# Kernel tuning notes

Hardware: AMD Instinct MI355X
Metric: run time of the kernel (lower is better)

The kernel has to match this reference:

```python
import jax, jax.numpy as jnp
import numpy as np

BITS = 8
EPS = 1e-08


def _scalar_quantize_maxabs(x, scale, bits, eps):
    # clamp(round(x / scale), -qmax, qmax) with a fixed (precomputed) scalar scale
    qmax = float(2 ** (bits - 1) - 1)
    s = jnp.maximum(scale, eps)
    return jnp.clip(jnp.round(x / s), -qmax, qmax)


def setup_inputs() -> dict:
    key = jax.random.key(0)
    k1, k2, k3 = jax.random.split(key, 3)
    B, S, D_in, D_out = 4, 2048, 2048, 2048
    hidden_states = jax.random.normal(k1, (B, S, D_in), dtype=jnp.float32)
    # weight_quantized holds low-bit integer values stored as float (as produced by the quantizer)
    qmax = float(2 ** (BITS - 1) - 1)
    weight_quantized = jnp.round(
        jnp.clip(jax.random.normal(k2, (D_in, D_out), dtype=jnp.float32) * (qmax / 3.0), -qmax, qmax)
    )
    x_scale = jnp.asarray(0.05, dtype=jnp.float32)
    bias = jax.random.normal(k3, (D_out,), dtype=jnp.float32)
    return {
        "hidden_states": hidden_states,
        "weight_quantized": weight_quantized,
        "x_scale": x_scale,
        "bias": bias,
    }


def reference(hidden_states, weight_quantized, x_scale, bias) -> jnp.ndarray:
    original_shape = hidden_states.shape[:-1]
    input_dim = hidden_states.shape[-1]
    x_flat = hidden_states.reshape(-1, input_dim)  # [B*S, D_in]
    x_q = _scalar_quantize_maxabs(x_flat, x_scale.reshape(()), BITS, EPS)
    out = x_q.astype(weight_quantized.dtype) @ weight_quantized  # [B*S, D_out]
    out = out + bias.astype(out.dtype)[None, :]
    return out.astype(hidden_states.dtype).reshape(*original_shape, weight_quantized.shape[1])
```

## Files before the change

### kernel.cpp

```cpp
#include <hip/hip_runtime.h>
#include <cstdint>
#include <cstddef>

#define MDIM 8192
#define NDIM 2048
#define KDIM 2048

constexpr int BM = 128, BN = 128, BK = 64;

typedef int v4i __attribute__((ext_vector_type(4)));

__device__ __forceinline__ void async_ld16(const void* g, void* l) {
    __builtin_amdgcn_global_load_lds(
        (const __attribute__((address_space(1))) int*)g,
        (__attribute__((address_space(3))) int*)l,
        16, 0, 0);
}

__device__ __forceinline__ uint32_t q8(float x, float inv) {
    float q = fminf(fmaxf(rintf(x * inv), -127.f), 127.f);
    return (uint32_t)((int)q) & 0xffu;
}

__global__ void quant_x_kernel(const float4* __restrict__ x, uint32_t* __restrict__ xq,
                               const float* __restrict__ scale_p) {
    int i = blockIdx.x * blockDim.x + threadIdx.x;
    float inv = 1.0f / fmaxf(scale_p[0], 1e-8f);
    float4 v = x[i];
    xq[i] = q8(v.x, inv) | (q8(v.y, inv) << 8) | (q8(v.z, inv) << 16) | (q8(v.w, inv) << 24);
}

__global__ void quant_wt_kernel(const float* __restrict__ w, uint32_t* __restrict__ wt) {
    __shared__ uint32_t t[64][17];
    const int k0 = blockIdx.y * 64;
    const int n0 = blockIdx.x * 64;
    const int tid = threadIdx.x;
    const int rr  = tid >> 4;
    const int c4  = (tid & 15) * 4;
#pragma unroll
    for (int p = 0; p < 4; ++p) {
        int r = rr + p * 16;
        float4 v = *(const float4*)&w[(size_t)(k0 + r) * NDIM + n0 + c4];
        uint32_t pk = (uint32_t)((int)rintf(v.x) & 0xff)
                    | ((uint32_t)((int)rintf(v.y) & 0xff) << 8)
                    | ((uint32_t)((int)rintf(v.z) & 0xff) << 16)
                    | ((uint32_t)((int)rintf(v.w) & 0xff) << 24);
        t[r][c4 >> 2] = pk;
    }
    __syncthreads();
#pragma unroll
    for (int p = 0; p < 4; ++p) {
        int c = rr + p * 16;
        uint32_t o = 0;
#pragma unroll
        for (int j = 0; j < 4; ++j) {
            uint32_t b = (t[c4 + j][c >> 2] >> ((c & 3) * 8)) & 0xffu;
            o |= b << (j * 8);
        }
        wt[((size_t)(n0 + c) * KDIM + k0 + c4) >> 2] = o;
    }
}

__global__ __launch_bounds__(256, 4)
void gemm_i8_kernel(const int8_t* __restrict__ A,
                    const int8_t* __restrict__ Bt,
                    const float* __restrict__ bias,
                    float* __restrict__ C) {
    __shared__ alignas(16) int8_t lA[2][BM * BK];
    __shared__ alignas(16) int8_t lB[2][BN * BK];

    const int tid  = threadIdx.x;
    const int lane = tid & 63;
    const int wave = tid >> 6;
    const int wm   = wave & 1;
    const int wn   = wave >> 1;
    const int m0   = blockIdx.y * BM;
    const int n0   = blockIdx.x * BN;

    const int srow = lane >> 2;
    const int schk = (lane & 3) ^ ((srow >> 1) & 3);
    const int8_t* gA = A  + (size_t)(m0 + wave * 32 + srow) * KDIM + schk * 16;
    const int8_t* gB = Bt + (size_t)(n0 + wave * 32 + srow) * KDIM + schk * 16;
    const int lwo = wave * 2048;

    const int quad = lane >> 4;
    const int lr   = lane & 15;
    const int fchk = (quad ^ ((lr >> 1) & 3)) * 16;
    const int aoff = (wm * 64 + lr) * BK + fchk;
    const int boff = (wn * 64 + lr) * BK + fchk;

    v4i acc[4][4];
#pragma unroll
    for (int i = 0; i < 4; ++i)
#pragma unroll
        for (int j = 0; j < 4; ++j)
            acc[i][j] = (v4i){0, 0, 0, 0};

#define STAGE(buf, kof)                                                        \
    do {                                                                       \
        async_ld16(gA + (kof), &lA[buf][lwo]);                                 \
        async_ld16(gA + (kof) + (size_t)16 * KDIM, &lA[buf][lwo + 1024]);      \
        async_ld16(gB + (kof), &lB[buf][lwo]);                                 \
        async_ld16(gB + (kof) + (size_t)16 * KDIM, &lB[buf][lwo + 1024]);      \
    } while (0)

#define COMPUTE(buf)                                                           \
    do {                                                                       \
        v4i af[4], bf[4];                                                      \
        _Pragma("unroll")                                                      \
        for (int i = 0; i < 4; ++i)                                            \
            af[i] = *(const v4i*)&lA[buf][aoff + i * 16 * BK];                 \
        _Pragma("unroll")                                                      \
        for (int j = 0; j < 4; ++j)                                            \
            bf[j] = *(const v4i*)&lB[buf][boff + j * 16 * BK];                 \
        _Pragma("unroll")                                                      \
        for (int i = 0; i < 4; ++i)                                            \
            _Pragma("unroll")                                                  \
            for (int j = 0; j < 4; ++j)                                        \
                acc[i][j] = __builtin_amdgcn_mfma_i32_16x16x64_i8(             \
                    af[i], bf[j], acc[i][j], 0, 0, 0);                         \
    } while (0)

    STAGE(0, 0);
    int kof = BK;
    for (int it = 0; it < KDIM / BK - 1; ++it) {
        __syncthreads();
        STAGE((it + 1) & 1, kof);
        kof += BK;
        COMPUTE(it & 1);
    }
    __syncthreads();
    COMPUTE((KDIM / BK - 1) & 1);

    const int crow = m0 + wm * 64 + quad * 4;
    const int ccol = n0 + wn * 64 + lr;
    float bj[4];
#pragma unroll
    for (int j = 0; j < 4; ++j) bj[j] = bias[ccol + j * 16];
#pragma unroll
    for (int i = 0; i < 4; ++i)
#pragma unroll
        for (int j = 0; j < 4; ++j)
#pragma unroll
            for (int r = 0; r < 4; ++r)
                C[(size_t)(crow + i * 16 + r) * NDIM + (ccol + j * 16)] = (float)acc[i][j][r] + bj[j];
}

extern "C" void kernel_launch(void* const* d_in, const int* in_sizes, int n_in,
                              void* d_out, int out_size, void* d_ws, size_t ws_size,
                              hipStream_t stream) {
    const float* x    = (const float*)d_in[0];
    const float* w    = (const float*)d_in[1];
    const float* xs   = (const float*)d_in[2];
    const float* bias = (const float*)d_in[3];
    float* out = (float*)d_out;

    int8_t* xq = (int8_t*)d_ws;
    int8_t* wt = xq + (size_t)MDIM * KDIM;

    quant_x_kernel<<<((size_t)MDIM * KDIM / 4) / 256, 256, 0, stream>>>(
        (const float4*)x, (uint32_t*)xq, xs);
    quant_wt_kernel<<<dim3(NDIM / 64, KDIM / 64), 256, 0, stream>>>(w, (uint32_t*)wt);
    gemm_i8_kernel<<<dim3(NDIM / BN, MDIM / BM), 256, 0, stream>>>(xq, wt, bias, out);
}
```

Before: 169.3 us.

## Enlarge GEMM tiles to 256x256 with 4-stage async pipeline and fuse quant kernels

Doubles the block tile to 256x256 with 512 threads and 8 M-fragments per wave, raising arithmetic intensity per LDS/global byte. Replaces the double buffer with a 4-deep ring using explicit vmcnt waits and barriers, plus MFMA priority hints. Adds a block-index swizzle for L2 locality and merges the two quantization kernels into one launch. It costs higher register and LDS use (128 KB), leaving one block per CU and a single wave of 256 blocks.

```diff
diff --git a/kernel.cpp b/kernel.cpp
--- a/kernel.cpp
+++ b/kernel.cpp
@@ -6,7 +6,9 @@
 #define NDIM 2048
 #define KDIM 2048
 
-constexpr int BM = 128, BN = 128, BK = 64;
+constexpr int BM = 256, BN = 256, BK = 64;
+constexpr int NT = KDIM / BK;
+constexpr int NBUF = 4;
 
 typedef int v4i __attribute__((ext_vector_type(4)));
 
@@ -22,19 +24,25 @@
     return (uint32_t)((int)q) & 0xffu;
 }
 
-__global__ void quant_x_kernel(const float4* __restrict__ x, uint32_t* __restrict__ xq,
-                               const float* __restrict__ scale_p) {
-    int i = blockIdx.x * blockDim.x + threadIdx.x;
-    float inv = 1.0f / fmaxf(scale_p[0], 1e-8f);
-    float4 v = x[i];
-    xq[i] = q8(v.x, inv) | (q8(v.y, inv) << 8) | (q8(v.z, inv) << 16) | (q8(v.w, inv) << 24);
-}
+#define XBLOCKS (MDIM * KDIM / 4 / 256)
 
-__global__ void quant_wt_kernel(const float* __restrict__ w, uint32_t* __restrict__ wt) {
+__global__ void quant_kernel(const float4* __restrict__ x, uint32_t* __restrict__ xq,
+                             const float* __restrict__ scale_p,
+                             const float* __restrict__ w, uint32_t* __restrict__ wt) {
     __shared__ uint32_t t[64][17];
-    const int k0 = blockIdx.y * 64;
-    const int n0 = blockIdx.x * 64;
     const int tid = threadIdx.x;
+
+    if (blockIdx.x < XBLOCKS) {
+        int i = blockIdx.x * 256 + tid;
+        float inv = 1.0f / fmaxf(scale_p[0], 1e-8f);
+        float4 v = x[i];
+        xq[i] = q8(v.x, inv) | (q8(v.y, inv) << 8) | (q8(v.z, inv) << 16) | (q8(v.w, inv) << 24);
+        return;
+    }
+
+    const int bid = blockIdx.x - XBLOCKS;
+    const int k0 = (bid >> 5) * 64;
+    const int n0 = (bid & 31) * 64;
     const int rr  = tid >> 4;
     const int c4  = (tid & 15) * 4;
 #pragma unroll
@@ -61,21 +69,24 @@
     }
 }
 
-__global__ __launch_bounds__(256, 4)
+__global__ __launch_bounds__(512, 2)
 void gemm_i8_kernel(const int8_t* __restrict__ A,
                     const int8_t* __restrict__ Bt,
                     const float* __restrict__ bias,
                     float* __restrict__ C) {
-    __shared__ alignas(16) int8_t lA[2][BM * BK];
-    __shared__ alignas(16) int8_t lB[2][BN * BK];
+    __shared__ alignas(16) int8_t lA[NBUF][BM * BK];
+    __shared__ alignas(16) int8_t lB[NBUF][BN * BK];
 
     const int tid  = threadIdx.x;
     const int lane = tid & 63;
     const int wave = tid >> 6;
     const int wm   = wave & 1;
     const int wn   = wave >> 1;
-    const int m0   = blockIdx.y * BM;
-    const int n0   = blockIdx.x * BN;
+
+    const int bidlin = blockIdx.y * gridDim.x + blockIdx.x;
+    const int swz    = (bidlin & 7) * 32 + (bidlin >> 3);
+    const int m0     = (swz >> 3) * BM;
+    const int n0     = (swz & 7) * BN;
 
     const int srow = lane >> 2;
     const int schk = (lane & 3) ^ ((srow >> 1) & 3);
@@ -86,12 +97,12 @@
     const int quad = lane >> 4;
     const int lr   = lane & 15;
     const int fchk = (quad ^ ((lr >> 1) & 3)) * 16;
-    const int aoff = (wm * 64 + lr) * BK + fchk;
+    const int aoff = (wm * 128 + lr) * BK + fchk;
     const int boff = (wn * 64 + lr) * BK + fchk;
 
-    v4i acc[4][4];
+    v4i acc[8][4];
 #pragma unroll
-    for (int i = 0; i < 4; ++i)
+    for (int i = 0; i < 8; ++i)
 #pragma unroll
         for (int j = 0; j < 4; ++j)
             acc[i][j] = (v4i){0, 0, 0, 0};
@@ -106,39 +117,58 @@
 
 #define COMPUTE(buf)                                                           \
     do {                                                                       \
-        v4i af[4], bf[4];                                                      \
-        _Pragma("unroll")                                                      \
-        for (int i = 0; i < 4; ++i)                                            \
-            af[i] = *(const v4i*)&lA[buf][aoff + i * 16 * BK];                 \
+        v4i bf[4];                                                             \
         _Pragma("unroll")                                                      \
         for (int j = 0; j < 4; ++j)                                            \
-            bf[j] = *(const v4i*)&lB[buf][boff + j * 16 * BK];                 \
+            bf[j] = *(const v4i*)&lB[buf][boff + j * 1024];                    \
+        __builtin_amdgcn_s_setprio(1);                                         \
         _Pragma("unroll")                                                      \
-        for (int i = 0; i < 4; ++i)                                            \
+        for (int i = 0; i < 8; ++i) {                                          \
+            v4i af = *(const v4i*)&lA[buf][aoff + i * 1024];                   \
             _Pragma("unroll")                                                  \
             for (int j = 0; j < 4; ++j)                                        \
                 acc[i][j] = __builtin_amdgcn_mfma_i32_16x16x64_i8(             \
-                    af[i], bf[j], acc[i][j], 0, 0, 0);                         \
+                    af, bf[j], acc[i][j], 0, 0, 0);                            \
+        }                                                                      \
+        __builtin_amdgcn_s_setprio(0);                                        \
+    } while (0)
+
+#define WAITBAR(n)                                                             \
+    do {                                                                       \
+        asm volatile("s_waitcnt vmcnt(" #n ")" ::: "memory");                  \
+        __builtin_amdgcn_s_barrier();                                          \
+        asm volatile("" ::: "memory");                                         \
     } while (0)
 
     STAGE(0, 0);
-    int kof = BK;
-    for (int it = 0; it < KDIM / BK - 1; ++it) {
-        __syncthreads();
-        STAGE((it + 1) & 1, kof);
+    STAGE(1, BK);
+    STAGE(2, 2 * BK);
+
+    int kof = 3 * BK;
+    for (int t = 0; t < NT - 3; ++t) {
+        WAITBAR(8);
+        STAGE((t + 3) & 3, kof);
         kof += BK;
-        COMPUTE(it & 1);
+        COMPUTE(t & 3);
     }
-    __syncthreads();
-    COMPUTE((KDIM / BK - 1) & 1);
+    WAITBAR(8);
+    COMPUTE((NT - 3) & 3);
+    WAITBAR(4);
+    COMPUTE((NT - 2) & 3);
+    WAITBAR(0);
+    COMPUTE((NT - 1) & 3);
 
-    const int crow = m0 + wm * 64 + quad * 4;
+#undef STAGE
+#undef COMPUTE
+#undef WAITBAR
+
+    const int crow = m0 + wm * 128 + quad * 4;
     const int ccol = n0 + wn * 64 + lr;
     float bj[4];
 #pragma unroll
     for (int j = 0; j < 4; ++j) bj[j] = bias[ccol + j * 16];
 #pragma unroll
-    for (int i = 0; i < 4; ++i)
+    for (int i = 0; i < 8; ++i)
 #pragma unroll
         for (int j = 0; j < 4; ++j)
 #pragma unroll
@@ -158,8 +188,7 @@
     int8_t* xq = (int8_t*)d_ws;
     int8_t* wt = xq + (size_t)MDIM * KDIM;
 
-    quant_x_kernel<<<((size_t)MDIM * KDIM / 4) / 256, 256, 0, stream>>>(
-        (const float4*)x, (uint32_t*)xq, xs);
-    quant_wt_kernel<<<dim3(NDIM / 64, KDIM / 64), 256, 0, stream>>>(w, (uint32_t*)wt);
-    gemm_i8_kernel<<<dim3(NDIM / BN, MDIM / BM), 256, 0, stream>>>(xq, wt, bias, out);
+    quant_kernel<<<XBLOCKS + (KDIM / 64) * (NDIM / 64), 256, 0, stream>>>(
+        (const float4*)x, (uint32_t*)xq, xs, w, (uint32_t*)wt);
+    gemm_i8_kernel<<<dim3(NDIM / BN, MDIM / BM), 512, 0, stream>>>(xq, wt, bias, out);
 }
```

Measured after the change: 171.6 us. Within noise of the previous version (+1.4%).
